# Kernel optimization log

Measured on AMD Instinct MI355X. Metric: run time of the kernel, lower is better.

Reference implementation:

```python
import jax, jax.numpy as jnp
import numpy as np

NUM_TYPES = 8
NUM_TAGS = 1 + 2 * NUM_TYPES  # tag 0 = 'O', 2t+1 = 'B-t', 2t+2 = 'I-t'
NEG = -10000.0


def _bio_constraints(num_types):
    K = 1 + 2 * num_types
    allowed = np.zeros((K, K), dtype=np.float32)
    for i in range(K):
        for j in range(K):
            if j == 0 or (j % 2 == 1):  # to O or to B-y: always allowed
                allowed[i, j] = 1.0
            else:  # to I-y: only from B-y or I-y
                y = (j - 2) // 2
                if i in (2 * y + 1, 2 * y + 2):
                    allowed[i, j] = 1.0
    start = np.array([1.0 if (j == 0 or j % 2 == 1) else 0.0 for j in range(K)], dtype=np.float32)
    end = np.ones((K,), dtype=np.float32)  # BIO: any tag may end a sequence
    return allowed, start, end


def setup_inputs() -> dict:
    key = jax.random.key(0)
    ks = jax.random.split(key, 8)
    B, T, D, K = 64, 512, 1024, NUM_TAGS
    mlm_out = jax.random.normal(ks[0], (B, T, D), dtype=jnp.float32)
    lengths = jax.random.randint(ks[1], (B,), T // 4, T + 1)  # variable lengths >= 1
    mask = (jnp.arange(T)[None, :] < lengths[:, None])  # bool [B,T], left-padded-free
    gold = jax.random.randint(ks[2], (B, T), 0, K)
    W = jax.random.normal(ks[3], (D, K), dtype=jnp.float32) * 0.02
    b = jnp.zeros((K,), dtype=jnp.float32)
    transitions = jax.random.normal(ks[4], (K, K), dtype=jnp.float32) * 0.1
    start_trans = jax.random.normal(ks[5], (K,), dtype=jnp.float32) * 0.1
    end_trans = jax.random.normal(ks[6], (K,), dtype=jnp.float32) * 0.1
    ta, sa, ea = _bio_constraints(NUM_TYPES)
    return {"mlm_out": mlm_out, "mask": mask, "gold": gold, "W": W, "b": b,
            "transitions": transitions, "start_trans": start_trans, "end_trans": end_trans,
            "trans_allowed": jnp.asarray(ta), "start_allowed": jnp.asarray(sa), "end_allowed": jnp.asarray(ea)}


def reference(mlm_out, mask, gold, W, b, transitions, start_trans, end_trans,
              trans_allowed, start_allowed, end_allowed):
    logits = jnp.einsum('btd,dk->btk', mlm_out, W) + b  # [B,T,K]
    maskf = mask.astype(logits.dtype)
    B, T, K = logits.shape

    # ---- joint (numerator) score, AllenNLP semantics ----
    score = start_trans[gold[:, 0]]
    pair = transitions[gold[:, :-1], gold[:, 1:]]                       # [B,T-1]
    emit = jnp.take_along_axis(logits, gold[:, :, None], axis=2)[..., 0]  # [B,T]
    score = score + jnp.sum(pair * maskf[:, 1:], axis=1) + jnp.sum(emit[:, :-1] * maskf[:, :-1], axis=1)
    lengths = jnp.sum(mask.astype(jnp.int32), axis=1)
    last_tags = jnp.take_along_axis(gold, (lengths - 1)[:, None], axis=1)[:, 0]
    last_emit = jnp.take_along_axis(logits[:, -1, :], last_tags[:, None], axis=1)[:, 0]
    score = score + end_trans[last_tags] + last_emit * maskf[:, -1]

    # ---- partition function (forward algorithm, log-space scan over time) ----
    logits_t = jnp.swapaxes(logits, 0, 1)  # [T,B,K]
    mask_t = jnp.swapaxes(maskf, 0, 1)     # [T,B]
    alpha0 = start_trans + logits_t[0]

    def fstep(alpha, xs):
        emit_t, m = xs
        inner = alpha[:, :, None] + transitions[None] + emit_t[:, None, :]  # [B,K,K]
        new = jax.scipy.special.logsumexp(inner, axis=1)
        return jnp.where(m[:, None] > 0, new, alpha), None

    alphaT, _ = jax.lax.scan(fstep, alpha0, (logits_t[1:], mask_t[1:]))
    logZ = jax.scipy.special.logsumexp(alphaT + end_trans, axis=1)

    loss = -jnp.sum(score - logZ)  # loss_weight = 1.0

    # ---- Viterbi decode with BIO-constrained transitions ----
    ct = transitions * trans_allowed + NEG * (1.0 - trans_allowed)
    cs = start_trans * start_allowed + NEG * (1.0 - start_allowed)
    ce = end_trans * end_allowed + NEG * (1.0 - end_allowed)
    v0 = cs + logits_t[0]

    def vstep(v, xs):
        emit_t, m = xs
        inner = v[:, :, None] + ct[None]          # [B,K,K]
        bp = jnp.argmax(inner, axis=1)            # [B,K] best prev tag per next tag
        best = jnp.max(inner, axis=1) + emit_t
        return jnp.where(m[:, None] > 0, best, v), bp

    vT, bps = jax.lax.scan(vstep, v0, (logits_t[1:], mask_t[1:]))  # bps [T-1,B,K]
    last_tag = jnp.argmax(vT + ce, axis=1)  # [B]

    def btstep(tag, xs):
        bp, m = xs
        prev = jnp.take_along_axis(bp, tag[:, None], axis=1)[:, 0]
        prev = jnp.where(m > 0, prev, tag)  # padded steps: carry tag through
        return prev, tag

    first_tag, tags_rest = jax.lax.scan(btstep, last_tag, (bps, mask_t[1:]), reverse=True)
    pred = jnp.concatenate([first_tag[None], tags_rest], axis=0).swapaxes(0, 1)  # [B,T]
    pred = pred * mask.astype(pred.dtype)
    return logits, loss, pred
```

## Files before the change

kernel.cpp:

```cpp
#include <hip/hip_runtime.h>
#include <math.h>

#define KK 17
#define TT 512
#define DD 1024
#define NBATCH 64
#define NEGC -10000.0f
#define NINF -1e30f
#define EMS 516
#define WTS 520

__device__ __forceinline__ float wsum64(float v) {
#pragma unroll
  for (int s = 32; s >= 1; s >>= 1) v += __shfl_xor(v, s);
  return v;
}
__device__ __forceinline__ int wsum64i(int v) {
#pragma unroll
  for (int s = 32; s >= 1; s >>= 1) v += __shfl_xor(v, s);
  return v;
}
__device__ __forceinline__ float rl(float x, int i) {
  return __int_as_float(__builtin_amdgcn_readlane(__float_as_int(x), i));
}
__device__ __forceinline__ float dppsum(float v) {
  float t;
  t = __int_as_float(__builtin_amdgcn_update_dpp(0, __float_as_int(v), 0x111, 0xf, 0xf, true));  v += t;
  t = __int_as_float(__builtin_amdgcn_update_dpp(0, __float_as_int(v), 0x112, 0xf, 0xf, true));  v += t;
  t = __int_as_float(__builtin_amdgcn_update_dpp(0, __float_as_int(v), 0x114, 0xf, 0xf, true));  v += t;
  t = __int_as_float(__builtin_amdgcn_update_dpp(0, __float_as_int(v), 0x118, 0xf, 0xf, true));  v += t;
  t = __int_as_float(__builtin_amdgcn_update_dpp(0, __float_as_int(v), 0x142, 0xa, 0xf, false)); v += t;
  t = __int_as_float(__builtin_amdgcn_update_dpp(0, __float_as_int(v), 0x143, 0xc, 0xf, false)); v += t;
  return v;
}
#define MAX3(d, a, b, c) \
  asm("v_max3_f32 %0, %1, %2, %3" : "=v"(d) : "v"(a), "v"(b), "v"(c));

__global__ __launch_bounds__(512) void k_logits(const float* __restrict__ X,
                                                const float* __restrict__ W,
                                                const float* __restrict__ b,
                                                float* __restrict__ logits,
                                                float* __restrict__ lossp) {
  __shared__ __align__(16) float Wt[KK * WTS];
  const int tid = threadIdx.x;
  const int lane = tid & 63;
  const int wv = tid >> 6;
  if (blockIdx.x == 0 && tid == 0) *lossp = 0.f;
  const long r0 = (long)blockIdx.x * 32 + wv * 4;
  const float* x0 = X + r0 * DD;
  float a0[KK], a1[KK], a2[KK], a3[KK];
#pragma unroll
  for (int j = 0; j < KK; ++j) { a0[j] = 0.f; a1[j] = 0.f; a2[j] = 0.f; a3[j] = 0.f; }

  for (int half = 0; half < 2; ++half) {
    __syncthreads();
    {
      const float* wr = W + (size_t)(half * 512 + tid) * KK;
#pragma unroll
      for (int j = 0; j < KK; ++j) Wt[j * WTS + tid] = wr[j];
    }
    __syncthreads();
#pragma unroll
    for (int it = 0; it < 2; ++it) {
      const int k4 = it * 256 + lane * 4;
      const float* xp = x0 + half * 512 + k4;
      float4 xa = *reinterpret_cast<const float4*>(xp);
      float4 xb = *reinterpret_cast<const float4*>(xp + DD);
      float4 xc = *reinterpret_cast<const float4*>(xp + 2 * DD);
      float4 xd = *reinterpret_cast<const float4*>(xp + 3 * DD);
#pragma unroll
      for (int j = 0; j < KK; ++j) {
        float4 w = *reinterpret_cast<const float4*>(&Wt[j * WTS + k4]);
        a0[j] = fmaf(xa.x, w.x, a0[j]); a0[j] = fmaf(xa.y, w.y, a0[j]);
        a0[j] = fmaf(xa.z, w.z, a0[j]); a0[j] = fmaf(xa.w, w.w, a0[j]);
        a1[j] = fmaf(xb.x, w.x, a1[j]); a1[j] = fmaf(xb.y, w.y, a1[j]);
        a1[j] = fmaf(xb.z, w.z, a1[j]); a1[j] = fmaf(xb.w, w.w, a1[j]);
        a2[j] = fmaf(xc.x, w.x, a2[j]); a2[j] = fmaf(xc.y, w.y, a2[j]);
        a2[j] = fmaf(xc.z, w.z, a2[j]); a2[j] = fmaf(xc.w, w.w, a2[j]);
        a3[j] = fmaf(xd.x, w.x, a3[j]); a3[j] = fmaf(xd.y, w.y, a3[j]);
        a3[j] = fmaf(xd.z, w.z, a3[j]); a3[j] = fmaf(xd.w, w.w, a3[j]);
      }
    }
  }
#pragma unroll
  for (int j = 0; j < KK; ++j) {
    a0[j] = dppsum(a0[j]); a1[j] = dppsum(a1[j]);
    a2[j] = dppsum(a2[j]); a3[j] = dppsum(a3[j]);
  }
  float v0 = 0.f, v1 = 0.f, v2 = 0.f, v3 = 0.f;
#pragma unroll
  for (int j = 0; j < KK; ++j) {
    float s0 = rl(a0[j], 63), s1 = rl(a1[j], 63), s2 = rl(a2[j], 63), s3 = rl(a3[j], 63);
    if (lane == j) { v0 = s0; v1 = s1; v2 = s2; v3 = s3; }
  }
  if (lane < KK) {
    float bb = b[lane];
    logits[r0 * KK + lane] = v0 + bb;
    logits[(r0 + 1) * KK + lane] = v1 + bb;
    logits[(r0 + 2) * KK + lane] = v2 + bb;
    logits[(r0 + 3) * KK + lane] = v3 + bb;
  }
}

__global__ __launch_bounds__(256) void k_scan(
    const float* __restrict__ logits, const void* __restrict__ maskp,
    const int* __restrict__ gold, const float* __restrict__ trans,
    const float* __restrict__ st, const float* __restrict__ et,
    const float* __restrict__ ta, const float* __restrict__ sa,
    const float* __restrict__ ea, float* __restrict__ lossp,
    float* __restrict__ predp) {
  __shared__ __align__(16) float EMT[KK * EMS];
  __shared__ __align__(4) unsigned char Mk[512];
  __shared__ unsigned char BPt[511 * KK];
  __shared__ unsigned char G2t[256 * KK];
  __shared__ unsigned char G4t[128 * KK];
  __shared__ unsigned char G8t[64 * KK];
  __shared__ unsigned char PR[512];
  __shared__ float red[2];
  __shared__ int shlt;

  const int tid = threadIdx.x;
  const int lane = tid & 63;
  const int wv = tid >> 6;
  const int batch = blockIdx.x;
  const float* Lg = logits + (size_t)batch * TT * KK;

  const unsigned char* mb = (const unsigned char*)maskp;
  const bool m_is_i32 = (mb[1] == 0);

  {
    const float4* Lg4 = reinterpret_cast<const float4*>(Lg);
    for (int i = tid; i < (TT * KK) / 4; i += 256) {
      float4 v = Lg4[i];
      int n = i * 4;
      int t0 = n / KK, j0 = n - t0 * KK;
      float vv[4] = {v.x, v.y, v.z, v.w};
#pragma unroll
      for (int e = 0; e < 4; ++e) {
        int j = j0 + e, t = t0;
        if (j >= KK) { j -= KK; t += 1; }
        EMT[j * EMS + t] = vv[e];
      }
    }
    if (m_is_i32) {
      const int* mi = (const int*)maskp + batch * TT;
      for (int t2 = tid; t2 < TT; t2 += 256) Mk[t2] = (unsigned char)(mi[t2] != 0);
    } else {
      const unsigned char* mB = mb + batch * TT;
      for (int t2 = tid; t2 < TT; t2 += 256) Mk[t2] = (unsigned char)(mB[t2] != 0);
    }
  }
  __syncthreads();
  int len;
  {
    const unsigned int* Mku = reinterpret_cast<const unsigned int*>(Mk);
    unsigned int a = Mku[lane], b2 = Mku[64 + lane];
    int c = (int)(((a * 0x01010101u) >> 24) + ((b2 * 0x01010101u) >> 24));
    len = wsum64i(c);
  }

  const int jc = lane < KK ? lane : (KK - 1);
  const float* EMTrow = EMT + jc * EMS;

  if (wv == 0) {
    float ctv[KK];
#pragma unroll
    for (int i = 0; i < KK; ++i)
      ctv[i] = (ta[i * KK + jc] > 0.5f) ? trans[i * KK + jc] : NEGC;
    unsigned char* bpw = BPt + jc;
    const bool act = lane < KK;
    float4 A = *reinterpret_cast<const float4*>(EMTrow);
    float v = ((sa[jc] > 0.5f) ? st[jc] : NEGC) + A.x;
    int t = 1;

#define VSTEP(EMV)                                                        \
    {                                                                     \
      float c0 = rl(v, 0) + ctv[0], c1 = rl(v, 1) + ctv[1];               \
      float c2 = rl(v, 2) + ctv[2], c3 = rl(v, 3) + ctv[3];               \
      float c4 = rl(v, 4) + ctv[4], c5 = rl(v, 5) + ctv[5];               \
      float c6 = rl(v, 6) + ctv[6], c7 = rl(v, 7) + ctv[7];               \
      float c8 = rl(v, 8) + ctv[8], c9 = rl(v, 9) + ctv[9];               \
      float c10 = rl(v, 10) + ctv[10], c11 = rl(v, 11) + ctv[11];         \
      float c12 = rl(v, 12) + ctv[12], c13 = rl(v, 13) + ctv[13];         \
      float c14 = rl(v, 14) + ctv[14], c15 = rl(v, 15) + ctv[15];         \
      float c16 = rl(v, 16) + ctv[16];                                    \
      float x0, x1, x2, x3, x4, y0, y1, bv;                               \
      MAX3(x0, c0, c1, c2)   MAX3(x1, c3, c4, c5)                         \
      MAX3(x2, c6, c7, c8)   MAX3(x3, c9, c10, c11)                       \
      MAX3(x4, c12, c13, c14)                                             \
      MAX3(y0, x0, x1, x2)   MAX3(y1, x3, x4, c15)                        \
      MAX3(bv, y0, y1, c16)                                               \
      float vn = bv + (EMV);                                              \
      v = (t < len) ? vn : v;                                             \
      int bi = 16;                                                        \
      bi = (c15 == bv) ? 15 : bi; bi = (c14 == bv) ? 14 : bi;             \
      bi = (c13 == bv) ? 13 : bi; bi = (c12 == bv) ? 12 : bi;             \
      bi = (c11 == bv) ? 11 : bi; bi = (c10 == bv) ? 10 : bi;             \
      bi = (c9 == bv) ? 9 : bi;   bi = (c8 == bv) ? 8 : bi;               \
      bi = (c7 == bv) ? 7 : bi;   bi = (c6 == bv) ? 6 : bi;               \
      bi = (c5 == bv) ? 5 : bi;   bi = (c4 == bv) ? 4 : bi;               \
      bi = (c3 == bv) ? 3 : bi;   bi = (c2 == bv) ? 2 : bi;               \
      bi = (c1 == bv) ? 1 : bi;   bi = (c0 == bv) ? 0 : bi;               \
      if (act) bpw[0] = (unsigned char)bi;                                \
      bpw += KK;                                                          \
      ++t;                                                                \
    }

    for (int g = 0; g < 127; ++g) {
      float4 B = *reinterpret_cast<const float4*>(EMTrow + 4 * g + 4);
      VSTEP(A.y) VSTEP(A.z) VSTEP(A.w) VSTEP(B.x)
      A = B;
    }
    VSTEP(A.y) VSTEP(A.z) VSTEP(A.w)
#undef VSTEP

    float fv = v + ((ea[jc] > 0.5f) ? et[jc] : NEGC);
    float best = rl(fv, 0);
    int bidx = 0;
#pragma unroll
    for (int i = 1; i < KK; ++i) {
      float fi = rl(fv, i);
      bool tk = fi > best;
      best = tk ? fi : best;
      bidx = tk ? i : bidx;
    }
    if (tid == 0) shlt = bidx;
  } else if (wv == 1) {
    float Pcol[KK];
#pragma unroll
    for (int i = 0; i < KK; ++i) Pcol[i] = __expf(trans[i * KK + jc]);
    float4 A = *reinterpret_cast<const float4*>(EMTrow);
    float a0v = st[jc] + A.x;
    float m0 = rl(a0v, 0);
#pragma unroll
    for (int i = 1; i < KK; ++i) m0 = fmaxf(m0, rl(a0v, i));
    float qown = __expf(a0v - m0);
    float C = m0;
    float ee = __expf(A.y);
    int t = 1;

#define FSTEP(EMNEXT, DOREN)                                                   \
    {                                                                          \
      float q0 = rl(qown, 0), q1 = rl(qown, 1), q2 = rl(qown, 2);              \
      float q3 = rl(qown, 3), q4 = rl(qown, 4), q5 = rl(qown, 5);              \
      float q6 = rl(qown, 6), q7 = rl(qown, 7), q8 = rl(qown, 8);              \
      float q9 = rl(qown, 9), q10 = rl(qown, 10), q11 = rl(qown, 11);          \
      float q12 = rl(qown, 12), q13 = rl(qown, 13), q14 = rl(qown, 14);        \
      float q15 = rl(qown, 15), q16 = rl(qown, 16);                            \
      float da = fmaf(q0, Pcol[0], fmaf(q4, Pcol[4], fmaf(q8, Pcol[8],         \
                 fmaf(q12, Pcol[12], q16 * Pcol[16]))));                       \
      float db = fmaf(q1, Pcol[1], fmaf(q5, Pcol[5], fmaf(q9, Pcol[9],         \
                 q13 * Pcol[13])));                                            \
      float dc = fmaf(q2, Pcol[2], fmaf(q6, Pcol[6], fmaf(q10, Pcol[10],       \
                 q14 * Pcol[14])));                                            \
      float dd = fmaf(q3, Pcol[3], fmaf(q7, Pcol[7], fmaf(q11, Pcol[11],       \
                 q15 * Pcol[15])));                                            \
      float qn = ((da + db) + (dc + dd)) * ee;                                 \
      ee = __expf(EMNEXT);                                                     \
      float qs = (t < len) ? qn : qown;                                        \
      if (DOREN) {                                                             \
        float s0 = ((q0 + q1) + (q2 + q3)) + ((q4 + q5) + (q6 + q7));          \
        float s1 = ((q8 + q9) + (q10 + q11)) + ((q12 + q13) + (q14 + q15));    \
        float s = (s0 + s1) + q16;                                             \
        C += __logf(s);                                                        \
        qs *= (1.0f / s);                                                      \
      }                                                                        \
      qown = qs;                                                               \
      ++t;                                                                     \
    }

    for (int g = 0; g < 127; ++g) {
      float4 B = *reinterpret_cast<const float4*>(EMTrow + 4 * g + 4);
      FSTEP(A.z, false) FSTEP(A.w, false) FSTEP(B.x, false)
      FSTEP(B.y, (g & 1))
      A = B;
    }
    FSTEP(A.z, false) FSTEP(A.w, false) FSTEP(A.w, false)
#undef FSTEP

    float term = qown * __expf(et[jc]);
    float S = rl(term, 0);
#pragma unroll
    for (int i = 1; i < KK; ++i) S += rl(term, i);
    if (lane == 0) red[0] = C + __logf(S);
  } else if (wv == 2) {
    const int* gb = gold + batch * TT;
    float esum = 0.f, tsum = 0.f;
#pragma unroll
    for (int u = 0; u < 8; ++u) {
      int t = lane + 64 * u;
      int gt = gb[t];
      float mt = (float)Mk[t];
      esum += mt * EMT[gt * EMS + t];
      int tn = (t + 1 < TT) ? t + 1 : TT - 1;
      int gn = gb[tn];
      float mtr = (t + 1 < TT && Mk[t + 1]) ? 1.f : 0.f;
      tsum += mtr * trans[gt * KK + gn];
    }
    float ssum = wsum64(esum + tsum);
    if (lane == 0) red[1] = ssum + st[gb[0]] + et[gb[len - 1]];
  }
  __syncthreads();
  if (tid == 0) atomicAdd(lossp, red[0] - red[1]);

  const int lt = shlt;
  {
    int m = tid;
    int s1 = 2 * m + 1, s0b = 2 * m;
    bool u1 = (s1 < 511) && Mk[s1 + 1];
    bool u0 = Mk[s0b + 1] != 0;
#pragma unroll
    for (int x = 0; x < KK; ++x) {
      int y = u1 ? (int)BPt[s1 * KK + x] : x;
      int z = u0 ? (int)BPt[s0b * KK + y] : y;
      G2t[m * KK + x] = (unsigned char)z;
    }
  }
  __syncthreads();
  if (tid < 128) {
    int p = tid;
#pragma unroll
    for (int x = 0; x < KK; ++x) {
      int y = G2t[(2 * p + 1) * KK + x];
      G4t[p * KK + x] = G2t[2 * p * KK + y];
    }
  }
  __syncthreads();
  if (tid < 64) {
    int p = tid;
#pragma unroll
    for (int x = 0; x < KK; ++x) {
      int y = G4t[(2 * p + 1) * KK + x];
      G8t[p * KK + x] = G4t[2 * p * KK + y];
    }
  }
  __syncthreads();
  if (tid == 0) {
    int x = lt;
    for (int p = 63; p >= 0; --p) {
      x = G8t[p * KK + x];
      PR[8 * p] = (unsigned char)x;
    }
  }
  __syncthreads();
  if (tid < 64) {
    int p = tid;
    int src = (p == 63) ? lt : (int)PR[8 * p + 8];
    PR[8 * p + 4] = G4t[(2 * p + 1) * KK + src];
  }
  __syncthreads();
  if (tid < 128) {
    int m = tid;
    int src = (m == 127) ? lt : (int)PR[4 * m + 4];
    PR[4 * m + 2] = G2t[(2 * m + 1) * KK + src];
  }
  __syncthreads();
  {
    int m = tid;
    int s = 2 * m + 1;
    int src = (m == 255) ? lt : (int)PR[2 * m + 2];
    int val = ((s < 511) && Mk[s + 1]) ? (int)BPt[s * KK + src] : src;
    PR[2 * m + 1] = (unsigned char)val;
  }
  __syncthreads();
  float* po = predp + batch * TT;
  for (int t2 = tid; t2 < TT; t2 += 256) po[t2] = Mk[t2] ? (float)PR[t2] : 0.f;
}

extern "C" void kernel_launch(void* const* d_in, const int* in_sizes, int n_in,
                              void* d_out, int out_size, void* d_ws, size_t ws_size,
                              hipStream_t stream) {
  const float* mlm = (const float*)d_in[0];
  const void* mask = d_in[1];
  const int* gold = (const int*)d_in[2];
  const float* W = (const float*)d_in[3];
  const float* b = (const float*)d_in[4];
  const float* trans = (const float*)d_in[5];
  const float* st = (const float*)d_in[6];
  const float* et = (const float*)d_in[7];
  const float* ta = (const float*)d_in[8];
  const float* sa = (const float*)d_in[9];
  const float* ea = (const float*)d_in[10];

  float* out = (float*)d_out;
  float* logits = out;
  float* lossp = out + (size_t)NBATCH * TT * KK;
  float* predp = lossp + 1;

  k_logits<<<dim3(1024), dim3(512), 0, stream>>>(mlm, W, b, logits, lossp);
  k_scan<<<dim3(64), dim3(256), 0, stream>>>(logits, mask, gold, trans, st, et,
                                             ta, sa, ea, lossp, predp);
}
```

Baseline: 375.8 us.

## Decouple Viterbi backpointer argmax from serial scan via pipelined helper waves

The Viterbi wave now computes only the running max per step and writes its score vector into a 128-entry ring buffer in LDS. The two otherwise idle waves then compute the argmax backpointers for the previous 56-step chunk in parallel, with block barriers between chunks. The forward-algorithm wave is split into the same chunks. This removes the 16-compare argmax and the backpointer store from the serial critical path, at the cost of ten extra barriers, an LDS store per step, and the extra LDS for the score history.

Result: faster. 302.0 us (-19.6%).

```diff
diff --git a/kernel.cpp b/kernel.cpp
--- a/kernel.cpp
+++ b/kernel.cpp
@@ -33,8 +33,6 @@
   t = __int_as_float(__builtin_amdgcn_update_dpp(0, __float_as_int(v), 0x143, 0xc, 0xf, false)); v += t;
   return v;
 }
-#define MAX3(d, a, b, c) \
-  asm("v_max3_f32 %0, %1, %2, %3" : "=v"(d) : "v"(a), "v"(b), "v"(c));
 
 __global__ __launch_bounds__(512) void k_logits(const float* __restrict__ X,
                                                 const float* __restrict__ W,
@@ -102,6 +100,9 @@
   }
 }
 
+#define ARGM(vl, il, vr, ir, vo, io) \
+  { bool tk = (vr) > (vl); vo = tk ? (vr) : (vl); io = tk ? (ir) : (il); }
+
 __global__ __launch_bounds__(256) void k_scan(
     const float* __restrict__ logits, const void* __restrict__ maskp,
     const int* __restrict__ gold, const float* __restrict__ trans,
@@ -111,6 +112,8 @@
     float* __restrict__ predp) {
   __shared__ __align__(16) float EMT[KK * EMS];
   __shared__ __align__(4) unsigned char Mk[512];
+  __shared__ float VH[128 * KK];
+  __shared__ float CTL[KK * KK];
   __shared__ unsigned char BPt[511 * KK];
   __shared__ unsigned char G2t[256 * KK];
   __shared__ unsigned char G4t[128 * KK];
@@ -149,6 +152,8 @@
       const unsigned char* mB = mb + batch * TT;
       for (int t2 = tid; t2 < TT; t2 += 256) Mk[t2] = (unsigned char)(mB[t2] != 0);
     }
+    for (int i = tid; i < KK * KK; i += 256)
+      CTL[i] = (ta[i] > 0.5f) ? trans[i] : NEGC;
   }
   __syncthreads();
   int len;
@@ -162,85 +167,58 @@
   const int jc = lane < KK ? lane : (KK - 1);
   const float* EMTrow = EMT + jc * EMS;
 
+  float v = 0.f;
+  float ctv[KK];
+  float Pcol[KK];
+  float qown = 0.f, C = 0.f, ee = 0.f;
+  int t = 1;
+
   if (wv == 0) {
-    float ctv[KK];
-#pragma unroll
-    for (int i = 0; i < KK; ++i)
-      ctv[i] = (ta[i * KK + jc] > 0.5f) ? trans[i * KK + jc] : NEGC;
-    unsigned char* bpw = BPt + jc;
-    const bool act = lane < KK;
-    float4 A = *reinterpret_cast<const float4*>(EMTrow);
-    float v = ((sa[jc] > 0.5f) ? st[jc] : NEGC) + A.x;
-    int t = 1;
-
-#define VSTEP(EMV)                                                        \
-    {                                                                     \
-      float c0 = rl(v, 0) + ctv[0], c1 = rl(v, 1) + ctv[1];               \
-      float c2 = rl(v, 2) + ctv[2], c3 = rl(v, 3) + ctv[3];               \
-      float c4 = rl(v, 4) + ctv[4], c5 = rl(v, 5) + ctv[5];               \
-      float c6 = rl(v, 6) + ctv[6], c7 = rl(v, 7) + ctv[7];               \
-      float c8 = rl(v, 8) + ctv[8], c9 = rl(v, 9) + ctv[9];               \
-      float c10 = rl(v, 10) + ctv[10], c11 = rl(v, 11) + ctv[11];         \
-      float c12 = rl(v, 12) + ctv[12], c13 = rl(v, 13) + ctv[13];         \
-      float c14 = rl(v, 14) + ctv[14], c15 = rl(v, 15) + ctv[15];         \
-      float c16 = rl(v, 16) + ctv[16];                                    \
-      float x0, x1, x2, x3, x4, y0, y1, bv;                               \
-      MAX3(x0, c0, c1, c2)   MAX3(x1, c3, c4, c5)                         \
-      MAX3(x2, c6, c7, c8)   MAX3(x3, c9, c10, c11)                       \
-      MAX3(x4, c12, c13, c14)                                             \
-      MAX3(y0, x0, x1, x2)   MAX3(y1, x3, x4, c15)                        \
-      MAX3(bv, y0, y1, c16)                                               \
-      float vn = bv + (EMV);                                              \
-      v = (t < len) ? vn : v;                                             \
-      int bi = 16;                                                        \
-      bi = (c15 == bv) ? 15 : bi; bi = (c14 == bv) ? 14 : bi;             \
-      bi = (c13 == bv) ? 13 : bi; bi = (c12 == bv) ? 12 : bi;             \
-      bi = (c11 == bv) ? 11 : bi; bi = (c10 == bv) ? 10 : bi;             \
-      bi = (c9 == bv) ? 9 : bi;   bi = (c8 == bv) ? 8 : bi;               \
-      bi = (c7 == bv) ? 7 : bi;   bi = (c6 == bv) ? 6 : bi;               \
-      bi = (c5 == bv) ? 5 : bi;   bi = (c4 == bv) ? 4 : bi;               \
-      bi = (c3 == bv) ? 3 : bi;   bi = (c2 == bv) ? 2 : bi;               \
-      bi = (c1 == bv) ? 1 : bi;   bi = (c0 == bv) ? 0 : bi;               \
-      if (act) bpw[0] = (unsigned char)bi;                                \
-      bpw += KK;                                                          \
-      ++t;                                                                \
-    }
-
-    for (int g = 0; g < 127; ++g) {
-      float4 B = *reinterpret_cast<const float4*>(EMTrow + 4 * g + 4);
-      VSTEP(A.y) VSTEP(A.z) VSTEP(A.w) VSTEP(B.x)
-      A = B;
-    }
-    VSTEP(A.y) VSTEP(A.z) VSTEP(A.w)
-#undef VSTEP
-
-    float fv = v + ((ea[jc] > 0.5f) ? et[jc] : NEGC);
-    float best = rl(fv, 0);
-    int bidx = 0;
-#pragma unroll
-    for (int i = 1; i < KK; ++i) {
-      float fi = rl(fv, i);
-      bool tk = fi > best;
-      best = tk ? fi : best;
-      bidx = tk ? i : bidx;
-    }
-    if (tid == 0) shlt = bidx;
+#pragma unroll
+    for (int i = 0; i < KK; ++i) ctv[i] = CTL[i * KK + jc];
+    v = ((sa[jc] > 0.5f) ? st[jc] : NEGC) + EMTrow[0];
+    VH[jc] = v;
   } else if (wv == 1) {
-    float Pcol[KK];
 #pragma unroll
     for (int i = 0; i < KK; ++i) Pcol[i] = __expf(trans[i * KK + jc]);
-    float4 A = *reinterpret_cast<const float4*>(EMTrow);
-    float a0v = st[jc] + A.x;
+    float a0v = st[jc] + EMTrow[0];
     float m0 = rl(a0v, 0);
 #pragma unroll
     for (int i = 1; i < KK; ++i) m0 = fmaxf(m0, rl(a0v, i));
-    float qown = __expf(a0v - m0);
-    float C = m0;
-    float ee = __expf(A.y);
-    int t = 1;
-
-#define FSTEP(EMNEXT, DOREN)                                                   \
+    qown = __expf(a0v - m0);
+    C = m0;
+    ee = __expf(EMTrow[1]);
+  }
+
+#define VSTEP6                                                             \
+    {                                                                      \
+      float em = EMTrow[t];                                                \
+      float c0 = rl(v, 0) + ctv[0], c1 = rl(v, 1) + ctv[1];                \
+      float c2 = rl(v, 2) + ctv[2], c3 = rl(v, 3) + ctv[3];                \
+      float c4 = rl(v, 4) + ctv[4], c5 = rl(v, 5) + ctv[5];                \
+      float c6 = rl(v, 6) + ctv[6], c7 = rl(v, 7) + ctv[7];                \
+      float c8 = rl(v, 8) + ctv[8], c9 = rl(v, 9) + ctv[9];                \
+      float c10 = rl(v, 10) + ctv[10], c11 = rl(v, 11) + ctv[11];          \
+      float c12 = rl(v, 12) + ctv[12], c13 = rl(v, 13) + ctv[13];          \
+      float c14 = rl(v, 14) + ctv[14], c15 = rl(v, 15) + ctv[15];          \
+      float c16 = rl(v, 16) + ctv[16];                                     \
+      float m01 = fmaxf(c0, c1), m23 = fmaxf(c2, c3);                      \
+      float m45 = fmaxf(c4, c5), m67 = fmaxf(c6, c7);                      \
+      float m89 = fmaxf(c8, c9), mab = fmaxf(c10, c11);                    \
+      float mcd = fmaxf(c12, c13), mef = fmaxf(c14, c15);                  \
+      float n0 = fmaxf(m01, m23), n1 = fmaxf(m45, m67);                    \
+      float n2 = fmaxf(m89, mab), n3 = fmaxf(mcd, mef);                    \
+      float p0 = fmaxf(n0, n1), p1 = fmaxf(n2, n3);                        \
+      float bv = fmaxf(fmaxf(p0, p1), c16);                                \
+      float vn = bv + em;                                                  \
+      v = (t < len) ? vn : v;                                              \
+      VH[(t & 127) * KK + jc] = v;                                         \
+      ++t;                                                                 \
+    }
+
+#define FSTEP6(REN)                                                            \
     {                                                                          \
+      float en_raw = EMTrow[t + 1];                                            \
       float q0 = rl(qown, 0), q1 = rl(qown, 1), q2 = rl(qown, 2);              \
       float q3 = rl(qown, 3), q4 = rl(qown, 4), q5 = rl(qown, 5);              \
       float q6 = rl(qown, 6), q7 = rl(qown, 7), q8 = rl(qown, 8);              \
@@ -256,9 +234,9 @@
       float dd = fmaf(q3, Pcol[3], fmaf(q7, Pcol[7], fmaf(q11, Pcol[11],       \
                  q15 * Pcol[15])));                                            \
       float qn = ((da + db) + (dc + dd)) * ee;                                 \
-      ee = __expf(EMNEXT);                                                     \
+      ee = __expf(en_raw);                                                     \
       float qs = (t < len) ? qn : qown;                                        \
-      if (DOREN) {                                                             \
+      if (REN) {                                                               \
         float s0 = ((q0 + q1) + (q2 + q3)) + ((q4 + q5) + (q6 + q7));          \
         float s1 = ((q8 + q9) + (q10 + q11)) + ((q12 + q13) + (q14 + q15));    \
         float s = (s0 + s1) + q16;                                             \
@@ -269,39 +247,139 @@
       ++t;                                                                     \
     }
 
-    for (int g = 0; g < 127; ++g) {
-      float4 B = *reinterpret_cast<const float4*>(EMTrow + 4 * g + 4);
-      FSTEP(A.z, false) FSTEP(A.w, false) FSTEP(B.x, false)
-      FSTEP(B.y, (g & 1))
-      A = B;
-    }
-    FSTEP(A.z, false) FSTEP(A.w, false) FSTEP(A.w, false)
-#undef FSTEP
-
-    float term = qown * __expf(et[jc]);
-    float S = rl(term, 0);
-#pragma unroll
-    for (int i = 1; i < KK; ++i) S += rl(term, i);
-    if (lane == 0) red[0] = C + __logf(S);
-  } else if (wv == 2) {
-    const int* gb = gold + batch * TT;
-    float esum = 0.f, tsum = 0.f;
-#pragma unroll
-    for (int u = 0; u < 8; ++u) {
-      int t = lane + 64 * u;
-      int gt = gb[t];
-      float mt = (float)Mk[t];
-      esum += mt * EMT[gt * EMS + t];
-      int tn = (t + 1 < TT) ? t + 1 : TT - 1;
-      int gn = gb[tn];
-      float mtr = (t + 1 < TT && Mk[t + 1]) ? 1.f : 0.f;
-      tsum += mtr * trans[gt * KK + gn];
-    }
-    float ssum = wsum64(esum + tsum);
-    if (lane == 0) red[1] = ssum + st[gb[0]] + et[gb[len - 1]];
-  }
-  __syncthreads();
+  for (int k = 0; k < 10; ++k) {
+    if (wv == 0) {
+      if (k < 9) {
+#pragma unroll
+        for (int s2 = 0; s2 < 56; ++s2) VSTEP6
+      } else {
+#pragma unroll
+        for (int s2 = 0; s2 < 7; ++s2) VSTEP6
+      }
+    } else if (wv == 1) {
+      if (k < 9) {
+#pragma unroll
+        for (int g = 0; g < 7; ++g) {
+          FSTEP6(0) FSTEP6(0) FSTEP6(0) FSTEP6(0)
+          FSTEP6(0) FSTEP6(0) FSTEP6(0) FSTEP6(1)
+        }
+      } else {
+#pragma unroll
+        for (int s2 = 0; s2 < 7; ++s2) FSTEP6(0)
+        float term = qown * __expf(et[jc]);
+        float S = rl(term, 0);
+#pragma unroll
+        for (int i = 1; i < KK; ++i) S += rl(term, i);
+        if (lane == 0) red[0] = C + __logf(S);
+      }
+    } else {
+      if (k == 0) {
+        if (wv == 2) {
+          const int* gb = gold + batch * TT;
+          float esum = 0.f, tsum = 0.f;
+#pragma unroll
+          for (int u = 0; u < 8; ++u) {
+            int tg = lane + 64 * u;
+            int gt = gb[tg];
+            float mt = (float)Mk[tg];
+            esum += mt * EMT[gt * EMS + tg];
+            int tn = (tg + 1 < TT) ? tg + 1 : TT - 1;
+            int gn = gb[tn];
+            float mtr = (tg + 1 < TT && Mk[tg + 1]) ? 1.f : 0.f;
+            tsum += mtr * trans[gt * KK + gn];
+          }
+          float ssum = wsum64(esum + tsum);
+          if (lane == 0) red[1] = ssum + st[gb[0]] + et[gb[len - 1]];
+        }
+      } else {
+        const int sbase = 56 * (k - 1);
+        for (int n = tid - 128; n < 56 * KK; n += 128) {
+          int tl = (n * 61681) >> 20;
+          int j = n - tl * 17;
+          int s = sbase + tl;
+          const float* vr = &VH[(s & 127) * KK];
+          const float* ct = &CTL[j];
+          float c0 = vr[0] + ct[0];     float c1 = vr[1] + ct[17];
+          float c2 = vr[2] + ct[34];    float c3 = vr[3] + ct[51];
+          float c4 = vr[4] + ct[68];    float c5 = vr[5] + ct[85];
+          float c6 = vr[6] + ct[102];   float c7 = vr[7] + ct[119];
+          float c8 = vr[8] + ct[136];   float c9 = vr[9] + ct[153];
+          float c10 = vr[10] + ct[170]; float c11 = vr[11] + ct[187];
+          float c12 = vr[12] + ct[204]; float c13 = vr[13] + ct[221];
+          float c14 = vr[14] + ct[238]; float c15 = vr[15] + ct[255];
+          float c16 = vr[16] + ct[272];
+          float d0, d1, d2, d3, d4, d5, d6, d7;
+          int j0, j1, j2, j3, j4, j5, j6, j7;
+          ARGM(c0, 0, c1, 1, d0, j0)     ARGM(c2, 2, c3, 3, d1, j1)
+          ARGM(c4, 4, c5, 5, d2, j2)     ARGM(c6, 6, c7, 7, d3, j3)
+          ARGM(c8, 8, c9, 9, d4, j4)     ARGM(c10, 10, c11, 11, d5, j5)
+          ARGM(c12, 12, c13, 13, d6, j6) ARGM(c14, 14, c15, 15, d7, j7)
+          float e0, e1, e2, e3; int k0, k1, k2, k3;
+          ARGM(d0, j0, d1, j1, e0, k0)   ARGM(d2, j2, d3, j3, e1, k1)
+          ARGM(d4, j4, d5, j5, e2, k2)   ARGM(d6, j6, d7, j7, e3, k3)
+          float f0, f1; int l0, l1;
+          ARGM(e0, k0, e1, k1, f0, l0)   ARGM(e2, k2, e3, k3, f1, l1)
+          float g0; int m0i;
+          ARGM(f0, l0, f1, l1, g0, m0i)
+          float bvv; int bi;
+          ARGM(g0, m0i, c16, 16, bvv, bi)
+          BPt[s * KK + j] = (unsigned char)bi;
+        }
+      }
+    }
+    __syncthreads();
+  }
+#undef VSTEP6
+#undef FSTEP6
+
+  if (wv == 0) {
+    float fv = v + ((ea[jc] > 0.5f) ? et[jc] : NEGC);
+    float best = rl(fv, 0);
+    int bidx = 0;
+#pragma unroll
+    for (int i = 1; i < KK; ++i) {
+      float fi = rl(fv, i);
+      bool tk = fi > best;
+      best = tk ? fi : best;
+      bidx = tk ? i : bidx;
+    }
+    if (tid == 0) shlt = bidx;
+  } else if (wv >= 2) {
+    for (int n = tid - 128; n < 7 * KK; n += 128) {
+      int tl = (n * 61681) >> 20;
+      int j = n - tl * 17;
+      int s = 504 + tl;
+      const float* vr = &VH[(s & 127) * KK];
+      const float* ct = &CTL[j];
+      float c0 = vr[0] + ct[0];     float c1 = vr[1] + ct[17];
+      float c2 = vr[2] + ct[34];    float c3 = vr[3] + ct[51];
+      float c4 = vr[4] + ct[68];    float c5 = vr[5] + ct[85];
+      float c6 = vr[6] + ct[102];   float c7 = vr[7] + ct[119];
+      float c8 = vr[8] + ct[136];   float c9 = vr[9] + ct[153];
+      float c10 = vr[10] + ct[170]; float c11 = vr[11] + ct[187];
+      float c12 = vr[12] + ct[204]; float c13 = vr[13] + ct[221];
+      float c14 = vr[14] + ct[238]; float c15 = vr[15] + ct[255];
+      float c16 = vr[16] + ct[272];
+      float d0, d1, d2, d3, d4, d5, d6, d7;
+      int j0, j1, j2, j3, j4, j5, j6, j7;
+      ARGM(c0, 0, c1, 1, d0, j0)     ARGM(c2, 2, c3, 3, d1, j1)
+      ARGM(c4, 4, c5, 5, d2, j2)     ARGM(c6, 6, c7, 7, d3, j3)
+      ARGM(c8, 8, c9, 9, d4, j4)     ARGM(c10, 10, c11, 11, d5, j5)
+      ARGM(c12, 12, c13, 13, d6, j6) ARGM(c14, 14, c15, 15, d7, j7)
+      float e0, e1, e2, e3; int k0, k1, k2, k3;
+      ARGM(d0, j0, d1, j1, e0, k0)   ARGM(d2, j2, d3, j3, e1, k1)
+      ARGM(d4, j4, d5, j5, e2, k2)   ARGM(d6, j6, d7, j7, e3, k3)
+      float f0, f1; int l0, l1;
+      ARGM(e0, k0, e1, k1, f0, l0)   ARGM(e2, k2, e3, k3, f1, l1)
+      float g0; int m0i;
+      ARGM(f0, l0, f1, l1, g0, m0i)
+      float bvv; int bi;
+      ARGM(g0, m0i, c16, 16, bvv, bi)
+      BPt[s * KK + j] = (unsigned char)bi;
+    }
+  }
   if (tid == 0) atomicAdd(lossp, red[0] - red[1]);
+  __syncthreads();
 
   const int lt = shlt;
   {
```
